# Optimization experiments

Hardware: AMD Instinct MI355X
Metric: run time of the kernel (lower is better)

The kernel has to match this reference:

```python
import jax, jax.numpy as jnp
import numpy as np

NUM_HEADS = 16
HEAD_DIM = 64  # 1024 / 16


def setup_inputs() -> dict:
    key = jax.random.key(0)
    ks = jax.random.split(key, 8)
    B, S, D = 2, 2048, 1024
    s = 0.02
    return {
        "hidden_states_q": jax.random.normal(ks[0], (B, S, D), jnp.float32),
        "hidden_states_k": jax.random.normal(ks[1], (B, S, D), jnp.float32),
        "hidden_states_v": jax.random.normal(ks[2], (B, S, D), jnp.float32),
        "Wq": jax.random.normal(ks[3], (D, D), jnp.float32) * s,
        "bq": jnp.zeros((D,), jnp.float32),
        "Wk": jax.random.normal(ks[4], (D, D), jnp.float32) * s,
        "bk": jnp.zeros((D,), jnp.float32),
        "Wv": jax.random.normal(ks[5], (D, D), jnp.float32) * s,
        "bv": jnp.zeros((D,), jnp.float32),
        "Wp": jax.random.normal(ks[6], (D, D), jnp.float32) * s,
        "bp": jnp.zeros((D,), jnp.float32),
    }


def _split_heads(x):
    B, S, D = x.shape
    return x.reshape(B, S, NUM_HEADS, HEAD_DIM).transpose(0, 2, 1, 3)  # [B,H,S,dh]


def reference(hidden_states_q, hidden_states_k, hidden_states_v,
              Wq, bq, Wk, bk, Wv, bv, Wp, bp):
    # Projections (Linear / Conv1D are both x @ W + b in this parameterization)
    q = _split_heads(hidden_states_q @ Wq + bq)
    k = _split_heads(hidden_states_k @ Wk + bk)
    v = _split_heads(hidden_states_v @ Wv + bv)
    scale = 1.0 / jnp.sqrt(jnp.asarray(HEAD_DIM, q.dtype))
    # NOTE: no causal mask is applied in the original _attn (mask asserted None)
    attn = jnp.einsum("bhqd,bhkd->bhqk", q, k) * scale
    attn = jax.nn.softmax(attn, axis=-1)  # attn_dropout is identity in eval
    out = jnp.einsum("bhqk,bhkd->bhqd", attn, v)
    B, H, S, dh = out.shape
    out = out.transpose(0, 2, 1, 3).reshape(B, S, H * dh)
    out = out @ Wp + bp  # resid_dropout identity in eval
    return out
```

## Files before the change

kernel.cpp:

```cpp
#include <hip/hip_runtime.h>
#include <stdint.h>


typedef _Float16 f16;
typedef __attribute__((ext_vector_type(8))) _Float16 f16x8;
typedef __attribute__((ext_vector_type(4))) _Float16 f16x4;
typedef __attribute__((ext_vector_type(4))) float f32x4;
typedef __attribute__((ext_vector_type(16))) float f32x16;
typedef __attribute__((ext_vector_type(2))) unsigned u32x2;

#define NB 2
#define SEQ 2048
#define DMODEL 1024
#define NH 16
#define DH 64

#define QSCALE 0.1803368801111601f

__device__ __forceinline__ void gload_lds16(const void* g, void* l) {
  __builtin_amdgcn_global_load_lds(
      (const __attribute__((address_space(1))) unsigned int*)g,
      (__attribute__((address_space(3))) unsigned int*)l, 16, 0, 0);
}

__device__ __forceinline__ void plswap(unsigned& a, unsigned& b) {
  u32x2 r = __builtin_amdgcn_permlane32_swap(a, b, false, false);
  a = r[0];
  b = r[1];
}

__global__ __launch_bounds__(256) void cast_f16_3(
    const float* __restrict__ s0, const float* __restrict__ s1,
    const float* __restrict__ s2, f16* __restrict__ d0, f16* __restrict__ d1,
    f16* __restrict__ d2) {
  const float* src = blockIdx.z == 0 ? s0 : (blockIdx.z == 1 ? s1 : s2);
  f16* dst = blockIdx.z == 0 ? d0 : (blockIdx.z == 1 ? d1 : d2);
  int i = (blockIdx.x * 256 + threadIdx.x) * 8;
  float4 a = *(const float4*)(src + i);
  float4 b = *(const float4*)(src + i + 4);
  f16x8 o;
  o[0] = (f16)a.x; o[1] = (f16)a.y; o[2] = (f16)a.z; o[3] = (f16)a.w;
  o[4] = (f16)b.x; o[5] = (f16)b.y; o[6] = (f16)b.z; o[7] = (f16)b.w;
  *(f16x8*)(dst + i) = o;
}

__global__ __launch_bounds__(256) void transw(
    const float* __restrict__ w0, const float* __restrict__ w1,
    const float* __restrict__ w2, const float* __restrict__ w3,
    f16* __restrict__ t0, f16* __restrict__ t1, f16* __restrict__ t2,
    f16* __restrict__ t3) {
  __shared__ float tile[64][65];
  const float* W; f16* T;
  switch (blockIdx.z) {
    case 0: W = w0; T = t0; break;
    case 1: W = w1; T = t1; break;
    case 2: W = w2; T = t2; break;
    default: W = w3; T = t3; break;
  }
  int r0 = blockIdx.y * 64, c0 = blockIdx.x * 64;
  for (int it = 0; it < 16; ++it) {
    int idx = it * 256 + threadIdx.x;
    int r = idx >> 6, c = idx & 63;
    tile[r][c] = W[(size_t)(r0 + r) * DMODEL + c0 + c];
  }
  __syncthreads();
  for (int it = 0; it < 16; ++it) {
    int idx = it * 256 + threadIdx.x;
    int r = idx >> 6, c = idx & 63;
    T[(size_t)(c0 + r) * DMODEL + r0 + c] = (f16)tile[c][r];
  }
}

__global__ __launch_bounds__(256) void gemm128(
    const f16* __restrict__ xq, const f16* __restrict__ xk,
    const f16* __restrict__ xv, const f16* __restrict__ ao,
    const f16* __restrict__ wqt, const f16* __restrict__ wkt,
    const f16* __restrict__ wvt, const f16* __restrict__ wpt,
    const float* __restrict__ bq, const float* __restrict__ bk,
    const float* __restrict__ bv, const float* __restrict__ bp,
    f16* __restrict__ qo, f16* __restrict__ ko, f16* __restrict__ vto,
    float* __restrict__ out, int mode_base) {
  __shared__ char lds[32768];
  char* ldsA = lds;
  char* ldsB = lds + 16384;

  int mode = mode_base + blockIdx.z;
  const f16* Am; const f16* Bt; const float* bias; float oscale = 1.0f;
  if (mode == 0)      { Am = xq; Bt = wqt; bias = bq; oscale = QSCALE; }
  else if (mode == 1) { Am = xk; Bt = wkt; bias = bk; }
  else if (mode == 2) { Am = xv; Bt = wvt; bias = bv; }
  else                { Am = ao; Bt = wpt; bias = bp; }

  const int tid = threadIdx.x;
  const int l = tid & 63, w = tid >> 6;
  const int g = l >> 4, c = l & 15;
  const int wr = w >> 1, wc = w & 1;
  const int m0 = blockIdx.y * 128, n0 = blockIdx.x * 128;

  const int srow = w * 8 + (l >> 3);
  const int schunk = (l & 7) ^ ((l >> 3) & 7);

  f32x4 acc[4][4] = {};

  for (int k0 = 0; k0 < DMODEL; k0 += 64) {
#pragma unroll
    for (int it = 0; it < 4; ++it) {
      int row = it * 32 + srow;
      gload_lds16(Am + (size_t)(m0 + row) * DMODEL + k0 + schunk * 8,
                  ldsA + it * 4096 + w * 1024);
    }
#pragma unroll
    for (int it = 0; it < 4; ++it) {
      int row = it * 32 + srow;
      gload_lds16(Bt + (size_t)(n0 + row) * DMODEL + k0 + schunk * 8,
                  ldsB + it * 4096 + w * 1024);
    }
    __syncthreads();
    f16x8 af[2][4], bf[2][4];
#pragma unroll
    for (int kc = 0; kc < 2; ++kc)
#pragma unroll
      for (int i = 0; i < 4; ++i) {
        int row = wr * 64 + i * 16 + c;
        af[kc][i] = *(const f16x8*)(ldsA + row * 128 + (((kc * 4 + g) ^ (row & 7)) << 4));
        int rowb = wc * 64 + i * 16 + c;
        bf[kc][i] = *(const f16x8*)(ldsB + rowb * 128 + (((kc * 4 + g) ^ (rowb & 7)) << 4));
      }
#pragma unroll
    for (int kc = 0; kc < 2; ++kc)
#pragma unroll
      for (int i = 0; i < 4; ++i)
#pragma unroll
        for (int j = 0; j < 4; ++j)
          acc[i][j] = __builtin_amdgcn_mfma_f32_16x16x32_f16(af[kc][i], bf[kc][j],
                                                             acc[i][j], 0, 0, 0);
    __syncthreads();
  }

#pragma unroll
  for (int i = 0; i < 4; ++i) {
#pragma unroll
    for (int j = 0; j < 4; ++j) {
      int grb = m0 + wr * 64 + i * 16 + g * 4;
      int gc = n0 + wc * 64 + j * 16 + c;
      float bval = bias[gc];
      if (mode == 3) {
#pragma unroll
        for (int e = 0; e < 4; ++e)
          out[(size_t)(grb + e) * DMODEL + gc] = acc[i][j][e] + bval;
      } else if (mode == 2) {
        int b = grb >> 11, s = grb & 2047, h = gc >> 6, d = gc & 63;
        f16x4 pk;
#pragma unroll
        for (int e = 0; e < 4; ++e) pk[e] = (f16)(acc[i][j][e] + bval);
        *(f16x4*)(vto + ((size_t)((b * NH + h) * DH + d)) * SEQ + s) = pk;
      } else {
        f16* dst = (mode == 0) ? qo : ko;
        int b = grb >> 11, s = grb & 2047, h = gc >> 6, d = gc & 63;
#pragma unroll
        for (int e = 0; e < 4; ++e)
          dst[(((size_t)(b * NH + h) * SEQ) + (s + e)) * DH + d] =
              (f16)((acc[i][j][e] + bval) * oscale);
      }
    }
  }
}

__global__ __launch_bounds__(256, 4) void attn64(
    const f16* __restrict__ qg, const f16* __restrict__ kg,
    const f16* __restrict__ vtg, f16* __restrict__ aout) {
  __shared__ char lds[32768];

  const int tid = threadIdx.x;
  const int l = tid & 63, w = tid >> 6;
  const int q31 = l & 31;
  const bool hi = l >= 32;
  const int p = w & 1;
  const int qgrp = w >> 1;

  const int bid = blockIdx.x;
  const int bh = (bid & 7) + 8 * (bid >> 8);
  const int qc = (bid >> 3) & 31;
  const int q0 = qc * 64 + qgrp * 32;

  f16x8 qf[4];
#pragma unroll
  for (int ks = 0; ks < 4; ++ks)
    qf[ks] = *(const f16x8*)(qg + ((size_t)bh * SEQ + q0 + q31) * DH + ks * 16 +
                             (hi ? 8 : 0));

  float lsum = 0.0f;
  f32x16 oacc[2] = {};

  const int srow = w * 8 + (l >> 3);
  const int schunk = (l & 7) ^ ((l >> 3) & 7);

  auto stage = [&](int buf, int t) {
    char* baseK = lds + buf * 16384;
    char* baseV = baseK + 8192;
#pragma unroll
    for (int it = 0; it < 2; ++it) {
      int row = it * 32 + srow;
      gload_lds16(kg + ((size_t)bh * SEQ + t * 64 + row) * DH + schunk * 8,
                  baseK + it * 4096 + w * 1024);
      gload_lds16(vtg + ((size_t)bh * DH + row) * SEQ + t * 64 + schunk * 8,
                  baseV + it * 4096 + w * 1024);
    }
  };

  stage(0, 0);

  for (int t = 0; t < 32; ++t) {
    int cur = t & 1;
    if (t + 1 < 32) {
      stage(cur ^ 1, t + 1);
      asm volatile("s_waitcnt vmcnt(4)" ::: "memory");
    } else {
      asm volatile("s_waitcnt vmcnt(0)" ::: "memory");
    }
    __builtin_amdgcn_s_barrier();
    __builtin_amdgcn_sched_barrier(0);

    const char* ldsK = lds + cur * 16384;
    const char* ldsV = ldsK + 8192;

    f32x16 st = {};
    __builtin_amdgcn_s_setprio(1);
#pragma unroll
    for (int ks = 0; ks < 4; ++ks) {
      int row = p * 32 + q31;
      int ch = ((ks * 2 + (hi ? 1 : 0)) ^ (q31 & 7)) << 4;
      f16x8 kf = *(const f16x8*)(ldsK + row * 128 + ch);
      st = __builtin_amdgcn_mfma_f32_32x32x16_f16(kf, qf[ks], st, 0, 0, 0);
    }
    __builtin_amdgcn_s_setprio(0);

    float ps[16];
#pragma unroll
    for (int r = 0; r < 16; ++r) ps[r] = exp2f(st[r]);
    {
      float t0 = (ps[0] + ps[1]) + (ps[2] + ps[3]);
      float t1 = (ps[4] + ps[5]) + (ps[6] + ps[7]);
      float t2 = (ps[8] + ps[9]) + (ps[10] + ps[11]);
      float t3 = (ps[12] + ps[13]) + (ps[14] + ps[15]);
      lsum += (t0 + t1) + (t2 + t3);
    }
    unsigned dw[8];
#pragma unroll
    for (int i = 0; i < 8; ++i)
      dw[i] = __builtin_bit_cast(
          unsigned, __builtin_amdgcn_cvt_pkrtz(ps[2 * i], ps[2 * i + 1]));
    plswap(dw[0], dw[2]);
    plswap(dw[1], dw[3]);
    plswap(dw[4], dw[6]);
    plswap(dw[5], dw[7]);

    __builtin_amdgcn_s_setprio(1);
#pragma unroll
    for (int ks2 = 0; ks2 < 2; ++ks2) {
      union { unsigned u[4]; f16x8 v; } pb;
      pb.u[0] = dw[ks2 * 4 + 0];
      pb.u[1] = dw[ks2 * 4 + 1];
      pb.u[2] = dw[ks2 * 4 + 2];
      pb.u[3] = dw[ks2 * 4 + 3];
#pragma unroll
      for (int dt = 0; dt < 2; ++dt) {
        int vrow = dt * 32 + q31;
        int ch = ((p * 4 + ks2 * 2 + (hi ? 1 : 0)) ^ (vrow & 7)) << 4;
        f16x8 vf = *(const f16x8*)(ldsV + vrow * 128 + ch);
        oacc[dt] = __builtin_amdgcn_mfma_f32_32x32x16_f16(vf, pb.v, oacc[dt], 0, 0, 0);
      }
    }
    __builtin_amdgcn_s_setprio(0);
    __builtin_amdgcn_sched_barrier(0);
    __builtin_amdgcn_s_barrier();
  }

  char* reg = lds + qgrp * 9216;
  if (p == 1) {
#pragma unroll
    for (int j = 0; j < 8; ++j) {
      f32x4 ck;
#pragma unroll
      for (int e = 0; e < 4; ++e) ck[e] = oacc[j >> 2][(j & 3) * 4 + e];
      *(f32x4*)(reg + j * 1024 + l * 16) = ck;
    }
    *(float*)(reg + 8192 + l * 4) = lsum;
  }
  __syncthreads();
  if (p == 0) {
#pragma unroll
    for (int j = 0; j < 8; ++j) {
      f32x4 ck = *(const f32x4*)(reg + j * 1024 + l * 16);
#pragma unroll
      for (int e = 0; e < 4; ++e) oacc[j >> 2][(j & 3) * 4 + e] += ck[e];
    }
    float lt = lsum + *(const float*)(reg + 8192 + l * 4);
    lt += __shfl_xor(lt, 32);
    float inv = 1.0f / lt;
    const int b = bh >> 4, h = bh & 15;
    const int s = q0 + q31;
#pragma unroll
    for (int dt = 0; dt < 2; ++dt)
#pragma unroll
      for (int rg = 0; rg < 4; ++rg) {
        f16x4 pk;
#pragma unroll
        for (int j = 0; j < 4; ++j) pk[j] = (f16)(oacc[dt][rg * 4 + j] * inv);
        int d0 = dt * 32 + rg * 8 + (hi ? 4 : 0);
        *(f16x4*)(aout + ((size_t)(b * SEQ + s)) * DMODEL + h * DH + d0) = pk;
      }
  }
}

extern "C" void kernel_launch(void* const* d_in, const int* in_sizes, int n_in,
                              void* d_out, int out_size, void* d_ws, size_t ws_size,
                              hipStream_t stream) {
  const float* hq = (const float*)d_in[0];
  const float* hk = (const float*)d_in[1];
  const float* hv = (const float*)d_in[2];
  const float* Wq = (const float*)d_in[3];
  const float* bq = (const float*)d_in[4];
  const float* Wk = (const float*)d_in[5];
  const float* bk = (const float*)d_in[6];
  const float* Wv = (const float*)d_in[7];
  const float* bv = (const float*)d_in[8];
  const float* Wp = (const float*)d_in[9];
  const float* bp = (const float*)d_in[10];
  float* out = (float*)d_out;

  f16* xq  = (f16*)d_ws;
  f16* xk  = xq + 4194304;
  f16* xv  = xk + 4194304;
  f16* wqt = xv + 4194304;
  f16* wkt = wqt + 1048576;
  f16* wvt = wkt + 1048576;
  f16* wpt = wvt + 1048576;
  f16* qb  = wpt + 1048576;
  f16* kb  = qb + 4194304;
  f16* vtb = kb + 4194304;
  f16* ao  = vtb + 4194304;

  cast_f16_3<<<dim3(2048, 1, 3), 256, 0, stream>>>(hq, hk, hv, xq, xk, xv);
  transw<<<dim3(16, 16, 4), 256, 0, stream>>>(Wq, Wk, Wv, Wp, wqt, wkt, wvt, wpt);
  gemm128<<<dim3(8, 32, 3), 256, 0, stream>>>(xq, xk, xv, ao, wqt, wkt, wvt, wpt,
                                              bq, bk, bv, bp, qb, kb, vtb, out, 0);
  attn64<<<dim3(1024), 256, 0, stream>>>(qb, kb, vtb, ao);
  gemm128<<<dim3(8, 32, 1), 256, 0, stream>>>(xq, xk, xv, ao, wqt, wkt, wvt, wpt,
                                              bq, bk, bv, bp, qb, kb, vtb, out, 3);
}
```

Before: 155.7 us.

## Fuse input fp32-to-fp16 cast into projection GEMM and double attention query tile

Removes the separate cast kernel: the QKV projection GEMM now loads fp32 activations straight into registers, converts them to fp16 and writes them into swizzled LDS. This avoids writing and rereading fp16 copies of the inputs, at the cost of synchronous register loads instead of async global-to-LDS copies. Separately, the attention kernel now has each wave process 64 query rows (two 32-row fragments) per staged K/V tile, with half as many blocks. This raises K/V reuse from LDS but increases register pressure and lowers the occupancy bound from 4 to 2.

```diff
diff --git a/kernel.cpp b/kernel.cpp
--- a/kernel.cpp
+++ b/kernel.cpp
@@ -27,21 +27,6 @@
   u32x2 r = __builtin_amdgcn_permlane32_swap(a, b, false, false);
   a = r[0];
   b = r[1];
-}
-
-__global__ __launch_bounds__(256) void cast_f16_3(
-    const float* __restrict__ s0, const float* __restrict__ s1,
-    const float* __restrict__ s2, f16* __restrict__ d0, f16* __restrict__ d1,
-    f16* __restrict__ d2) {
-  const float* src = blockIdx.z == 0 ? s0 : (blockIdx.z == 1 ? s1 : s2);
-  f16* dst = blockIdx.z == 0 ? d0 : (blockIdx.z == 1 ? d1 : d2);
-  int i = (blockIdx.x * 256 + threadIdx.x) * 8;
-  float4 a = *(const float4*)(src + i);
-  float4 b = *(const float4*)(src + i + 4);
-  f16x8 o;
-  o[0] = (f16)a.x; o[1] = (f16)a.y; o[2] = (f16)a.z; o[3] = (f16)a.w;
-  o[4] = (f16)b.x; o[5] = (f16)b.y; o[6] = (f16)b.z; o[7] = (f16)b.w;
-  *(f16x8*)(dst + i) = o;
 }
 
 __global__ __launch_bounds__(256) void transw(
@@ -72,8 +57,8 @@
 }
 
 __global__ __launch_bounds__(256) void gemm128(
-    const f16* __restrict__ xq, const f16* __restrict__ xk,
-    const f16* __restrict__ xv, const f16* __restrict__ ao,
+    const float* __restrict__ hq, const float* __restrict__ hk,
+    const float* __restrict__ hv, const f16* __restrict__ ao,
     const f16* __restrict__ wqt, const f16* __restrict__ wkt,
     const f16* __restrict__ wvt, const f16* __restrict__ wpt,
     const float* __restrict__ bq, const float* __restrict__ bk,
@@ -85,11 +70,11 @@
   char* ldsB = lds + 16384;
 
   int mode = mode_base + blockIdx.z;
-  const f16* Am; const f16* Bt; const float* bias; float oscale = 1.0f;
-  if (mode == 0)      { Am = xq; Bt = wqt; bias = bq; oscale = QSCALE; }
-  else if (mode == 1) { Am = xk; Bt = wkt; bias = bk; }
-  else if (mode == 2) { Am = xv; Bt = wvt; bias = bv; }
-  else                { Am = ao; Bt = wpt; bias = bp; }
+  const float* Af; const f16* Bt; const float* bias; float oscale = 1.0f;
+  if (mode == 0)      { Af = hq; Bt = wqt; bias = bq; oscale = QSCALE; }
+  else if (mode == 1) { Af = hk; Bt = wkt; bias = bk; }
+  else if (mode == 2) { Af = hv; Bt = wvt; bias = bv; }
+  else                { Af = nullptr; Bt = wpt; bias = bp; }
 
   const int tid = threadIdx.x;
   const int l = tid & 63, w = tid >> 6;
@@ -100,14 +85,35 @@
   const int srow = w * 8 + (l >> 3);
   const int schunk = (l & 7) ^ ((l >> 3) & 7);
 
+  const int arow_base = w * 4 + (l >> 4);
+  const int akb = (l & 15);
+
   f32x4 acc[4][4] = {};
 
   for (int k0 = 0; k0 < DMODEL; k0 += 64) {
-#pragma unroll
-    for (int it = 0; it < 4; ++it) {
-      int row = it * 32 + srow;
-      gload_lds16(Am + (size_t)(m0 + row) * DMODEL + k0 + schunk * 8,
-                  ldsA + it * 4096 + w * 1024);
+    if (mode < 3) {
+      f32x4 av[8];
+#pragma unroll
+      for (int rr = 0; rr < 8; ++rr) {
+        int row = rr * 16 + arow_base;
+        av[rr] = *(const f32x4*)(Af + (size_t)(m0 + row) * DMODEL + k0 + akb * 4);
+      }
+#pragma unroll
+      for (int rr = 0; rr < 8; ++rr) {
+        int row = rr * 16 + arow_base;
+        f16x4 h4;
+        h4[0] = (f16)av[rr][0]; h4[1] = (f16)av[rr][1];
+        h4[2] = (f16)av[rr][2]; h4[3] = (f16)av[rr][3];
+        *(f16x4*)(ldsA + row * 128 + (((akb >> 1) ^ (row & 7)) << 4) +
+                  (akb & 1) * 8) = h4;
+      }
+    } else {
+#pragma unroll
+      for (int it = 0; it < 4; ++it) {
+        int row = it * 32 + srow;
+        gload_lds16(ao + (size_t)(m0 + row) * DMODEL + k0 + schunk * 8,
+                    ldsA + it * 4096 + w * 1024);
+      }
     }
 #pragma unroll
     for (int it = 0; it < 4; ++it) {
@@ -166,10 +172,10 @@
   }
 }
 
-__global__ __launch_bounds__(256, 4) void attn64(
+__global__ __launch_bounds__(256, 2) void attn64(
     const f16* __restrict__ qg, const f16* __restrict__ kg,
     const f16* __restrict__ vtg, f16* __restrict__ aout) {
-  __shared__ char lds[32768];
+  __shared__ char lds[33792];
 
   const int tid = threadIdx.x;
   const int l = tid & 63, w = tid >> 6;
@@ -179,18 +185,21 @@
   const int qgrp = w >> 1;
 
   const int bid = blockIdx.x;
-  const int bh = (bid & 7) + 8 * (bid >> 8);
-  const int qc = (bid >> 3) & 31;
-  const int q0 = qc * 64 + qgrp * 32;
-
-  f16x8 qf[4];
-#pragma unroll
-  for (int ks = 0; ks < 4; ++ks)
-    qf[ks] = *(const f16x8*)(qg + ((size_t)bh * SEQ + q0 + q31) * DH + ks * 16 +
-                             (hi ? 8 : 0));
-
-  float lsum = 0.0f;
-  f32x16 oacc[2] = {};
+  const int bh = (bid & 7) + 8 * (bid >> 7);
+  const int qc = (bid >> 3) & 15;
+  const int q0 = qc * 128 + qgrp * 64;
+
+  f16x8 qf0[4], qf1[4];
+#pragma unroll
+  for (int ks = 0; ks < 4; ++ks) {
+    qf0[ks] = *(const f16x8*)(qg + ((size_t)bh * SEQ + q0 + q31) * DH + ks * 16 +
+                              (hi ? 8 : 0));
+    qf1[ks] = *(const f16x8*)(qg + ((size_t)bh * SEQ + q0 + 32 + q31) * DH +
+                              ks * 16 + (hi ? 8 : 0));
+  }
+
+  float lsum0 = 0.0f, lsum1 = 0.0f;
+  f32x16 oacc00 = {}, oacc01 = {}, oacc10 = {}, oacc11 = {};
 
   const int srow = w * 8 + (l >> 3);
   const int schunk = (l & 7) ^ ((l >> 3) & 7);
@@ -206,6 +215,27 @@
       gload_lds16(vtg + ((size_t)bh * DH + row) * SEQ + t * 64 + schunk * 8,
                   baseV + it * 4096 + w * 1024);
     }
+  };
+
+  auto softmax = [&](const f32x16& st, float& lsum, unsigned* dw) {
+    float ps[16];
+#pragma unroll
+    for (int r = 0; r < 16; ++r) ps[r] = exp2f(st[r]);
+    {
+      float t0 = (ps[0] + ps[1]) + (ps[2] + ps[3]);
+      float t1 = (ps[4] + ps[5]) + (ps[6] + ps[7]);
+      float t2 = (ps[8] + ps[9]) + (ps[10] + ps[11]);
+      float t3 = (ps[12] + ps[13]) + (ps[14] + ps[15]);
+      lsum += (t0 + t1) + (t2 + t3);
+    }
+#pragma unroll
+    for (int i = 0; i < 8; ++i)
+      dw[i] = __builtin_bit_cast(
+          unsigned, __builtin_amdgcn_cvt_pkrtz(ps[2 * i], ps[2 * i + 1]));
+    plswap(dw[0], dw[2]);
+    plswap(dw[1], dw[3]);
+    plswap(dw[4], dw[6]);
+    plswap(dw[5], dw[7]);
   };
 
   stage(0, 0);
@@ -224,51 +254,43 @@
     const char* ldsK = lds + cur * 16384;
     const char* ldsV = ldsK + 8192;
 
-    f32x16 st = {};
+    f32x16 st0 = {}, st1 = {};
     __builtin_amdgcn_s_setprio(1);
 #pragma unroll
     for (int ks = 0; ks < 4; ++ks) {
       int row = p * 32 + q31;
       int ch = ((ks * 2 + (hi ? 1 : 0)) ^ (q31 & 7)) << 4;
       f16x8 kf = *(const f16x8*)(ldsK + row * 128 + ch);
-      st = __builtin_amdgcn_mfma_f32_32x32x16_f16(kf, qf[ks], st, 0, 0, 0);
+      st0 = __builtin_amdgcn_mfma_f32_32x32x16_f16(kf, qf0[ks], st0, 0, 0, 0);
+      st1 = __builtin_amdgcn_mfma_f32_32x32x16_f16(kf, qf1[ks], st1, 0, 0, 0);
     }
     __builtin_amdgcn_s_setprio(0);
 
-    float ps[16];
-#pragma unroll
-    for (int r = 0; r < 16; ++r) ps[r] = exp2f(st[r]);
-    {
-      float t0 = (ps[0] + ps[1]) + (ps[2] + ps[3]);
-      float t1 = (ps[4] + ps[5]) + (ps[6] + ps[7]);
-      float t2 = (ps[8] + ps[9]) + (ps[10] + ps[11]);
-      float t3 = (ps[12] + ps[13]) + (ps[14] + ps[15]);
-      lsum += (t0 + t1) + (t2 + t3);
-    }
-    unsigned dw[8];
-#pragma unroll
-    for (int i = 0; i < 8; ++i)
-      dw[i] = __builtin_bit_cast(
-          unsigned, __builtin_amdgcn_cvt_pkrtz(ps[2 * i], ps[2 * i + 1]));
-    plswap(dw[0], dw[2]);
-    plswap(dw[1], dw[3]);
-    plswap(dw[4], dw[6]);
-    plswap(dw[5], dw[7]);
+    unsigned dw0[8], dw1[8];
+    softmax(st0, lsum0, dw0);
+    softmax(st1, lsum1, dw1);
 
     __builtin_amdgcn_s_setprio(1);
 #pragma unroll
     for (int ks2 = 0; ks2 < 2; ++ks2) {
-      union { unsigned u[4]; f16x8 v; } pb;
-      pb.u[0] = dw[ks2 * 4 + 0];
-      pb.u[1] = dw[ks2 * 4 + 1];
-      pb.u[2] = dw[ks2 * 4 + 2];
-      pb.u[3] = dw[ks2 * 4 + 3];
-#pragma unroll
-      for (int dt = 0; dt < 2; ++dt) {
-        int vrow = dt * 32 + q31;
+      union { unsigned u[4]; f16x8 v; } pb0, pb1;
+      pb0.u[0] = dw0[ks2 * 4 + 0]; pb0.u[1] = dw0[ks2 * 4 + 1];
+      pb0.u[2] = dw0[ks2 * 4 + 2]; pb0.u[3] = dw0[ks2 * 4 + 3];
+      pb1.u[0] = dw1[ks2 * 4 + 0]; pb1.u[1] = dw1[ks2 * 4 + 1];
+      pb1.u[2] = dw1[ks2 * 4 + 2]; pb1.u[3] = dw1[ks2 * 4 + 3];
+      {
+        int vrow = q31;
         int ch = ((p * 4 + ks2 * 2 + (hi ? 1 : 0)) ^ (vrow & 7)) << 4;
         f16x8 vf = *(const f16x8*)(ldsV + vrow * 128 + ch);
-        oacc[dt] = __builtin_amdgcn_mfma_f32_32x32x16_f16(vf, pb.v, oacc[dt], 0, 0, 0);
+        oacc00 = __builtin_amdgcn_mfma_f32_32x32x16_f16(vf, pb0.v, oacc00, 0, 0, 0);
+        oacc10 = __builtin_amdgcn_mfma_f32_32x32x16_f16(vf, pb1.v, oacc10, 0, 0, 0);
+      }
+      {
+        int vrow = 32 + q31;
+        int ch = ((p * 4 + ks2 * 2 + (hi ? 1 : 0)) ^ (vrow & 7)) << 4;
+        f16x8 vf = *(const f16x8*)(ldsV + vrow * 128 + ch);
+        oacc01 = __builtin_amdgcn_mfma_f32_32x32x16_f16(vf, pb0.v, oacc01, 0, 0, 0);
+        oacc11 = __builtin_amdgcn_mfma_f32_32x32x16_f16(vf, pb1.v, oacc11, 0, 0, 0);
       }
     }
     __builtin_amdgcn_s_setprio(0);
@@ -276,40 +298,60 @@
     __builtin_amdgcn_s_barrier();
   }
 
-  char* reg = lds + qgrp * 9216;
+  __builtin_amdgcn_s_barrier();
+  char* reg = lds + qgrp * 16896;
   if (p == 1) {
 #pragma unroll
     for (int j = 0; j < 8; ++j) {
-      f32x4 ck;
-#pragma unroll
-      for (int e = 0; e < 4; ++e) ck[e] = oacc[j >> 2][(j & 3) * 4 + e];
-      *(f32x4*)(reg + j * 1024 + l * 16) = ck;
-    }
-    *(float*)(reg + 8192 + l * 4) = lsum;
+      f32x4 c0, c1;
+#pragma unroll
+      for (int e = 0; e < 4; ++e) {
+        c0[e] = (j < 4) ? oacc00[j * 4 + e] : oacc01[(j - 4) * 4 + e];
+        c1[e] = (j < 4) ? oacc10[j * 4 + e] : oacc11[(j - 4) * 4 + e];
+      }
+      *(f32x4*)(reg + j * 1024 + l * 16) = c0;
+      *(f32x4*)(reg + 8192 + j * 1024 + l * 16) = c1;
+    }
+    *(float*)(reg + 16384 + l * 4) = lsum0;
+    *(float*)(reg + 16640 + l * 4) = lsum1;
   }
   __syncthreads();
   if (p == 0) {
 #pragma unroll
     for (int j = 0; j < 8; ++j) {
-      f32x4 ck = *(const f32x4*)(reg + j * 1024 + l * 16);
-#pragma unroll
-      for (int e = 0; e < 4; ++e) oacc[j >> 2][(j & 3) * 4 + e] += ck[e];
-    }
-    float lt = lsum + *(const float*)(reg + 8192 + l * 4);
-    lt += __shfl_xor(lt, 32);
-    float inv = 1.0f / lt;
+      f32x4 c0 = *(const f32x4*)(reg + j * 1024 + l * 16);
+      f32x4 c1 = *(const f32x4*)(reg + 8192 + j * 1024 + l * 16);
+#pragma unroll
+      for (int e = 0; e < 4; ++e) {
+        if (j < 4) { oacc00[j * 4 + e] += c0[e]; oacc10[j * 4 + e] += c1[e]; }
+        else       { oacc01[(j - 4) * 4 + e] += c0[e]; oacc11[(j - 4) * 4 + e] += c1[e]; }
+      }
+    }
+    float lt0 = lsum0 + *(const float*)(reg + 16384 + l * 4);
+    float lt1 = lsum1 + *(const float*)(reg + 16640 + l * 4);
+    lt0 += __shfl_xor(lt0, 32);
+    lt1 += __shfl_xor(lt1, 32);
+    float inv0 = 1.0f / lt0, inv1 = 1.0f / lt1;
     const int b = bh >> 4, h = bh & 15;
-    const int s = q0 + q31;
-#pragma unroll
-    for (int dt = 0; dt < 2; ++dt)
-#pragma unroll
-      for (int rg = 0; rg < 4; ++rg) {
-        f16x4 pk;
-#pragma unroll
-        for (int j = 0; j < 4; ++j) pk[j] = (f16)(oacc[dt][rg * 4 + j] * inv);
-        int d0 = dt * 32 + rg * 8 + (hi ? 4 : 0);
-        *(f16x4*)(aout + ((size_t)(b * SEQ + s)) * DMODEL + h * DH + d0) = pk;
-      }
+#pragma unroll
+    for (int f = 0; f < 2; ++f) {
+      float inv = f ? inv1 : inv0;
+      int s = q0 + f * 32 + q31;
+#pragma unroll
+      for (int dt = 0; dt < 2; ++dt)
+#pragma unroll
+        for (int rg = 0; rg < 4; ++rg) {
+          f16x4 pk;
+#pragma unroll
+          for (int j = 0; j < 4; ++j) {
+            float v = f ? (dt ? oacc11[rg * 4 + j] : oacc10[rg * 4 + j])
+                        : (dt ? oacc01[rg * 4 + j] : oacc00[rg * 4 + j]);
+            pk[j] = (f16)(v * inv);
+          }
+          int d0 = dt * 32 + rg * 8 + (hi ? 4 : 0);
+          *(f16x4*)(aout + ((size_t)(b * SEQ + s)) * DMODEL + h * DH + d0) = pk;
+        }
+    }
   }
 }
 
@@ -329,10 +371,7 @@
   const float* bp = (const float*)d_in[10];
   float* out = (float*)d_out;
 
-  f16* xq  = (f16*)d_ws;
-  f16* xk  = xq + 4194304;
-  f16* xv  = xk + 4194304;
-  f16* wqt = xv + 4194304;
+  f16* wqt = (f16*)d_ws;
   f16* wkt = wqt + 1048576;
   f16* wvt = wkt + 1048576;
   f16* wpt = wvt + 1048576;
@@ -341,11 +380,10 @@
   f16* vtb = kb + 4194304;
   f16* ao  = vtb + 4194304;
 
-  cast_f16_3<<<dim3(2048, 1, 3), 256, 0, stream>>>(hq, hk, hv, xq, xk, xv);
   transw<<<dim3(16, 16, 4), 256, 0, stream>>>(Wq, Wk, Wv, Wp, wqt, wkt, wvt, wpt);
-  gemm128<<<dim3(8, 32, 3), 256, 0, stream>>>(xq, xk, xv, ao, wqt, wkt, wvt, wpt,
+  gemm128<<<dim3(8, 32, 3), 256, 0, stream>>>(hq, hk, hv, ao, wqt, wkt, wvt, wpt,
                                               bq, bk, bv, bp, qb, kb, vtb, out, 0);
-  attn64<<<dim3(1024), 256, 0, stream>>>(qb, kb, vtb, ao);
-  gemm128<<<dim3(8, 32, 1), 256, 0, stream>>>(xq, xk, xv, ao, wqt, wkt, wvt, wpt,
+  attn64<<<dim3(512), 256, 0, stream>>>(qb, kb, vtb, ao);
+  gemm128<<<dim3(8, 32, 1), 256, 0, stream>>>(hq, hk, hv, ao, wqt, wkt, wvt, wpt,
                                               bq, bk, bv, bp, qb, kb, vtb, out, 3);
 }
```

New measurement: 171.1 us. 1.1x slower.
